# Optimization experiments

Hardware: AMD Instinct MI355X
Metric: run time of the kernel (lower is better)

Reference implementation:

```python
import jax, jax.numpy as jnp
import numpy as np

EMBED_DIM = 1024
HEADS = 16
HEAD_DIM = EMBED_DIM // HEADS


def setup_inputs() -> dict:
    key = jax.random.key(0)
    ks = jax.random.split(key, 9)
    D = EMBED_DIM
    s = 1.0 / np.sqrt(D)
    x = jax.random.normal(ks[0], (4, 2048, D), dtype=jnp.float32)
    Wq = jax.random.uniform(ks[1], (D, D), jnp.float32, -s, s)
    bq = jnp.zeros((D,), jnp.float32)
    Wk = jax.random.uniform(ks[2], (D, D), jnp.float32, -s, s)
    bk = jnp.zeros((D,), jnp.float32)
    Wv = jax.random.uniform(ks[3], (D, D), jnp.float32, -s, s)
    bv = jnp.zeros((D,), jnp.float32)
    Wo = jax.random.uniform(ks[4], (D, D), jnp.float32, -s, s)
    bo = jnp.zeros((D,), jnp.float32)
    gamma = jnp.ones((D,), jnp.float32)
    beta = jnp.zeros((D,), jnp.float32)
    return {"x": x, "Wq": Wq, "bq": bq, "Wk": Wk, "bk": bk,
            "Wv": Wv, "bv": bv, "Wo": Wo, "bo": bo,
            "gamma": gamma, "beta": beta}


def reference(x, Wq, bq, Wk, bk, Wv, bv, Wo, bo, gamma, beta):
    B, S, D = x.shape
    H, Dh = HEADS, HEAD_DIM
    # projections -> [B, H, S, Dh]
    q = (x @ Wq + bq).reshape(B, S, H, Dh).transpose(0, 2, 1, 3)
    k = (x @ Wk + bk).reshape(B, S, H, Dh).transpose(0, 2, 1, 3)
    v = (x @ Wv + bv).reshape(B, S, H, Dh).transpose(0, 2, 1, 3)
    scores = jnp.einsum('bhqd,bhkd->bhqk', q, k) / jnp.sqrt(jnp.float32(Dh))
    attn = jax.nn.softmax(scores, axis=-1)  # dropout is identity in eval
    ctx = jnp.einsum('bhqk,bhkd->bhqd', attn, v)
    ctx = ctx.transpose(0, 2, 1, 3).reshape(B, S, D)
    out = ctx @ Wo + bo
    # residual + LayerNorm (eps=1e-5, torch default)
    h = out + x
    mu = jnp.mean(h, axis=-1, keepdims=True)
    var = jnp.mean(jnp.square(h - mu), axis=-1, keepdims=True)
    return (h - mu) * jax.lax.rsqrt(var + 1e-5) * gamma + beta
```

## Files before the change

### kernel.cpp

```cpp
#include <hip/hip_runtime.h>
#include <hip/hip_bf16.h>
#include <stdint.h>

typedef short sh4 __attribute__((ext_vector_type(4)));
typedef short sh8 __attribute__((ext_vector_type(8)));
typedef float fl4 __attribute__((ext_vector_type(4)));
typedef float f32x4 __attribute__((ext_vector_type(4)));
typedef float f32x16 __attribute__((ext_vector_type(16)));
typedef uint32_t u32x4 __attribute__((ext_vector_type(4)));

static __device__ __forceinline__ short f2bf(float f) {
  union { float f; uint32_t u; } v;
  v.f = f;
  uint32_t r = v.u + 0x7fffu + ((v.u >> 16) & 1u);
  return (short)(r >> 16);
}

static __device__ __forceinline__ uint32_t cvt_pk_bf16(float a, float b) {
  uint32_t r;
  asm("v_cvt_pk_bf16_f32 %0, %1, %2" : "=v"(r) : "v"(a), "v"(b));
  return r;
}

static __device__ __forceinline__ void pl32swap(uint32_t& a, uint32_t& b) {
  asm volatile("v_permlane32_swap_b32 %0, %1" : "+v"(a), "+v"(b));
}

static __device__ __forceinline__ void gload_lds16(const void* g, void* l) {
  __builtin_amdgcn_global_load_lds((const __attribute__((address_space(1))) void*)g,
                                   (__attribute__((address_space(3))) void*)l, 16, 0, 0);
}

__global__ __launch_bounds__(256) void k_wt(const float* __restrict__ Wq, const float* __restrict__ Wk,
                                            const float* __restrict__ Wv, const float* __restrict__ Wo,
                                            short* __restrict__ Tq, short* __restrict__ Tk,
                                            short* __restrict__ Tv, short* __restrict__ To) {
  const float* W = blockIdx.z == 0 ? Wq : blockIdx.z == 1 ? Wk : blockIdx.z == 2 ? Wv : Wo;
  short* T = blockIdx.z == 0 ? Tq : blockIdx.z == 1 ? Tk : blockIdx.z == 2 ? Tv : To;
  __shared__ float tile[32][33];
  int n0 = blockIdx.x * 32, k0 = blockIdx.y * 32;
  int tx = threadIdx.x, ty = threadIdx.y;
#pragma unroll
  for (int p = 0; p < 4; p++) tile[ty + 8 * p][tx] = W[(size_t)(k0 + ty + 8 * p) * 1024 + n0 + tx];
  __syncthreads();
#pragma unroll
  for (int p = 0; p < 4; p++) T[(size_t)(n0 + ty + 8 * p) * 1024 + k0 + tx] = f2bf(tile[tx][ty + 8 * p]);
}

__global__ __launch_bounds__(256) void k_cvtx(const float* __restrict__ x, short* __restrict__ o) {
  int i = blockIdx.x * 256 + threadIdx.x;
  fl4 v = ((const fl4*)x)[i];
  sh4 r;
#pragma unroll
  for (int j = 0; j < 4; j++) r[j] = f2bf(v[j]);
  ((sh4*)o)[i] = r;
}

#define PIPE_LOOP(STAGE_BODY, COMPUTE_BODY, VM)                          \
  STAGE_BODY(0, 0);                                                      \
  STAGE_BODY(1, 1);                                                      \
  {                                                                      \
    int bufc = 0, bufs = 2;                                              \
    for (int it = 0; it < 32; it++) {                                    \
      if (it < 31)                                                       \
        asm volatile("s_waitcnt vmcnt(" VM ")" ::: "memory");            \
      else                                                               \
        asm volatile("s_waitcnt vmcnt(0)" ::: "memory");                 \
      __builtin_amdgcn_s_barrier();                                      \
      if (it + 2 < 32) { STAGE_BODY(it + 2, bufs); }                     \
      __builtin_amdgcn_sched_barrier(0);                                 \
      { int buf = bufc; COMPUTE_BODY }                                   \
      bufc = bufc == 2 ? 0 : bufc + 1;                                   \
      bufs = bufs == 2 ? 0 : bufs + 1;                                   \
      asm volatile("" ::: "memory");                                     \
    }                                                                    \
  }

__global__ __launch_bounds__(512, 4) void k_qk(const short* __restrict__ A, const short* __restrict__ WT2,
                                               const float* __restrict__ bq, const float* __restrict__ bk,
                                               short* __restrict__ Qo, short* __restrict__ Ko, float qscale) {
  __shared__ __align__(16) short As[3][256 * 32];
  __shared__ __align__(16) short Bs[3][128 * 32];
  const int xcd = blockIdx.x & 7, j = blockIdx.x >> 3;
  const int m0 = (j >> 1) * 256, n0 = (xcd * 2 + (j & 1)) * 128;
  const int sec = n0 >> 10;
  const float* bias = sec == 0 ? bq : bk;
  short* Out = sec == 0 ? Qo : Ko;
  const float scale = sec == 0 ? qscale : 1.f;
  const int t = threadIdx.x;
  const int lane = t & 63, w = t >> 6;
  const int wr = w >> 1, wc = w & 1;
  const int l15 = lane & 15, g = lane >> 4;
  f32x4 acc[4][4];
#pragma unroll
  for (int mi = 0; mi < 4; mi++)
#pragma unroll
    for (int ni = 0; ni < 4; ni++) acc[mi][ni] = (f32x4){0.f, 0.f, 0.f, 0.f};

#define QK_STAGE(kt, buf)                                                                     \
  {                                                                                           \
    int r0 = w * 32;                                                                          \
    _Pragma("unroll") for (int i = 0; i < 2; i++) {                                           \
      int row = r0 + i * 16 + (lane >> 2);                                                    \
      gload_lds16(&A[(size_t)(m0 + row) * 1024 + (kt) * 32 + (lane & 3) * 8],                 \
                  &As[buf][(r0 + i * 16) * 32]);                                              \
    }                                                                                         \
    int brow = w * 16 + (lane >> 2);                                                          \
    gload_lds16(&WT2[(size_t)(n0 + brow) * 1024 + (kt) * 32 + (lane & 3) * 8],                \
                &Bs[buf][(w * 16) * 32]);                                                     \
  }

#define QK_COMPUTE                                                                            \
  sh8 a[4], b[4];                                                                             \
  _Pragma("unroll") for (int i = 0; i < 4; i++)                                               \
      a[i] = *(sh8*)&As[buf][(wr * 64 + i * 16 + l15) * 32 + g * 8];                          \
  _Pragma("unroll") for (int i = 0; i < 4; i++)                                               \
      b[i] = *(sh8*)&Bs[buf][(wc * 64 + i * 16 + l15) * 32 + g * 8];                          \
  _Pragma("unroll") for (int mi = 0; mi < 4; mi++)                                            \
      _Pragma("unroll") for (int ni = 0; ni < 4; ni++)                                        \
          acc[mi][ni] = __builtin_amdgcn_mfma_f32_16x16x32_bf16(b[ni], a[mi], acc[mi][ni], 0, 0, 0);

  PIPE_LOOP(QK_STAGE, QK_COMPUTE, "3")

#pragma unroll
  for (int ni = 0; ni < 4; ni++) {
    int nbase = n0 + wc * 64 + ni * 16 + g * 4;
    int nn0 = nbase & 1023;
    fl4 bv4 = *(const fl4*)&bias[nn0];
    int h = nn0 >> 6, dh0 = nn0 & 63;
#pragma unroll
    for (int mi = 0; mi < 4; mi++) {
      int m = m0 + wr * 64 + mi * 16 + l15;
      int bb = m >> 11, s = m & 2047;
      uint2 dd;
      dd.x = cvt_pk_bf16((acc[mi][ni][0] + bv4[0]) * scale, (acc[mi][ni][1] + bv4[1]) * scale);
      dd.y = cvt_pk_bf16((acc[mi][ni][2] + bv4[2]) * scale, (acc[mi][ni][3] + bv4[3]) * scale);
      *(uint2*)&Out[(((size_t)bb * 16 + h) * 2048 + s) * 64 + dh0] = dd;
    }
  }
}

__global__ __launch_bounds__(256) void k_v(const short* __restrict__ A, const short* __restrict__ WTv,
                                           const float* __restrict__ bv, short* __restrict__ Vo) {
  __shared__ __align__(16) short As[3][128 * 32];
  __shared__ __align__(16) short Bs[3][128 * 32];
  const int xcd = blockIdx.x & 7, j = blockIdx.x >> 3;
  const int m0 = (xcd + 8 * (j & 7)) * 128, n0 = (j >> 3) * 128;
  const int t = threadIdx.x;
  const int lane = t & 63, w = t >> 6;
  const int wr = w >> 1, wc = w & 1;
  const int l15 = lane & 15, g = lane >> 4;
  f32x4 acc[4][4];
#pragma unroll
  for (int mi = 0; mi < 4; mi++)
#pragma unroll
    for (int ni = 0; ni < 4; ni++) acc[mi][ni] = (f32x4){0.f, 0.f, 0.f, 0.f};

#define V_STAGE(kt, buf)                                                                      \
  {                                                                                           \
    int r0 = w * 32;                                                                          \
    _Pragma("unroll") for (int i = 0; i < 2; i++) {                                           \
      int row = r0 + i * 16 + (lane >> 2);                                                    \
      gload_lds16(&A[(size_t)(m0 + row) * 1024 + (kt) * 32 + (lane & 3) * 8],                 \
                  &As[buf][(r0 + i * 16) * 32]);                                              \
      gload_lds16(&WTv[(size_t)(n0 + row) * 1024 + (kt) * 32 + (lane & 3) * 8],               \
                  &Bs[buf][(r0 + i * 16) * 32]);                                              \
    }                                                                                         \
  }

#define V_COMPUTE                                                                             \
  sh8 a[4], b[4];                                                                             \
  _Pragma("unroll") for (int i = 0; i < 4; i++)                                               \
      a[i] = *(sh8*)&As[buf][(wr * 64 + i * 16 + l15) * 32 + g * 8];                          \
  _Pragma("unroll") for (int i = 0; i < 4; i++)                                               \
      b[i] = *(sh8*)&Bs[buf][(wc * 64 + i * 16 + l15) * 32 + g * 8];                          \
  _Pragma("unroll") for (int mi = 0; mi < 4; mi++)                                            \
      _Pragma("unroll") for (int ni = 0; ni < 4; ni++)                                        \
          acc[mi][ni] = __builtin_amdgcn_mfma_f32_16x16x32_bf16(a[mi], b[ni], acc[mi][ni], 0, 0, 0);

  PIPE_LOOP(V_STAGE, V_COMPUTE, "4")

#pragma unroll
  for (int ni = 0; ni < 4; ni++) {
    int col = n0 + wc * 64 + ni * 16 + l15;
    int nn = col & 1023;
    float bvv = bv[nn];
    int h = nn >> 6, dh = nn & 63;
#pragma unroll
    for (int mi = 0; mi < 4; mi++) {
      int mr = m0 + wr * 64 + mi * 16 + g * 4;
      int bb = mr >> 11, s = mr & 2047;
      uint2 dd;
      dd.x = cvt_pk_bf16(acc[mi][ni][0] + bvv, acc[mi][ni][1] + bvv);
      dd.y = cvt_pk_bf16(acc[mi][ni][2] + bvv, acc[mi][ni][3] + bvv);
      *(uint2*)&Vo[(((size_t)bb * 16 + h) * 64 + dh) * 2048 + s] = dd;
    }
  }
}

__global__ __launch_bounds__(256) void k_oproj(const short* __restrict__ A, const short* __restrict__ BT,
                                               const float* __restrict__ bias, const float* __restrict__ X,
                                               float* __restrict__ Out) {
  __shared__ __align__(16) short As[3][128 * 32];
  __shared__ __align__(16) short Bs[3][128 * 32];
  const int xcd = blockIdx.x & 7, j = blockIdx.x >> 3;
  const int m0 = (xcd + 8 * (j & 7)) * 128, n0 = (j >> 3) * 128;
  const int t = threadIdx.x;
  const int lane = t & 63, w = t >> 6;
  const int wr = w >> 1, wc = w & 1;
  const int l15 = lane & 15, g = lane >> 4;
  f32x4 acc[4][4];
#pragma unroll
  for (int mi = 0; mi < 4; mi++)
#pragma unroll
    for (int ni = 0; ni < 4; ni++) acc[mi][ni] = (f32x4){0.f, 0.f, 0.f, 0.f};

#define O_STAGE(kt, buf)                                                                      \
  {                                                                                           \
    int r0 = w * 32;                                                                          \
    _Pragma("unroll") for (int i = 0; i < 2; i++) {                                           \
      int row = r0 + i * 16 + (lane >> 2);                                                    \
      gload_lds16(&A[(size_t)(m0 + row) * 1024 + (kt) * 32 + (lane & 3) * 8],                 \
                  &As[buf][(r0 + i * 16) * 32]);                                              \
      gload_lds16(&BT[(size_t)(n0 + row) * 1024 + (kt) * 32 + (lane & 3) * 8],                \
                  &Bs[buf][(r0 + i * 16) * 32]);                                              \
    }                                                                                         \
  }

#define O_COMPUTE                                                                             \
  sh8 a[4], b[4];                                                                             \
  _Pragma("unroll") for (int i = 0; i < 4; i++)                                               \
      a[i] = *(sh8*)&As[buf][(wr * 64 + i * 16 + l15) * 32 + g * 8];                          \
  _Pragma("unroll") for (int i = 0; i < 4; i++)                                               \
      b[i] = *(sh8*)&Bs[buf][(wc * 64 + i * 16 + l15) * 32 + g * 8];                          \
  _Pragma("unroll") for (int mi = 0; mi < 4; mi++)                                            \
      _Pragma("unroll") for (int ni = 0; ni < 4; ni++)                                        \
          acc[mi][ni] = __builtin_amdgcn_mfma_f32_16x16x32_bf16(b[ni], a[mi], acc[mi][ni], 0, 0, 0);

  PIPE_LOOP(O_STAGE, O_COMPUTE, "4")

#pragma unroll
  for (int ni = 0; ni < 4; ni++) {
    int nbase = n0 + wc * 64 + ni * 16 + g * 4;
    fl4 bv4 = *(const fl4*)&bias[nbase];
#pragma unroll
    for (int mi = 0; mi < 4; mi++) {
      int m = m0 + wr * 64 + mi * 16 + l15;
      fl4 xv = *(const fl4*)&X[(size_t)m * 1024 + nbase];
      fl4 r;
#pragma unroll
      for (int e = 0; e < 4; e++) r[e] = acc[mi][ni][e] + bv4[e] + xv[e];
      *(fl4*)&Out[(size_t)m * 1024 + nbase] = r;
    }
  }
}

__global__ __launch_bounds__(512, 4) void k_attn(const short* __restrict__ Q, const short* __restrict__ K,
                                                 const short* __restrict__ Vt, short* __restrict__ CTX) {
  const int nid = (blockIdx.x & 7) * 64 + (blockIdx.x >> 3);
  const int qbi = nid & 7, h = (nid >> 3) & 15, b = nid >> 7;
  const int q0 = qbi * 256;
  const size_t ho = (((size_t)b * 16 + h) * 2048) * 64;
  const short* Qh = Q + ho;
  const short* Kh = K + ho;
  const short* Vh = Vt + ho;
  __shared__ __align__(16) short Ks[3][8 * 512];
  __shared__ __align__(16) short Vs[4][8 * 512];
  const int t = threadIdx.x, lane = t & 63, w = t >> 6;
  const int l31 = lane & 31, hi = lane >> 5;

  sh8 qreg[4];
#pragma unroll
  for (int ks = 0; ks < 4; ks++)
    qreg[ks] = *(const sh8*)&Qh[(size_t)(q0 + w * 32 + l31) * 64 + ks * 16 + hi * 8];

  f32x16 zinit;
#pragma unroll
  for (int r = 0; r < 16; r++) zinit[r] = 0.f;

  f32x16 oc0 = zinit, oc1 = zinit;
  float l_s = 0.f;
  u32x4 pwp[4];

  auto stageK = [&](int kt, int buf) {
    gload_lds16(&Kh[(size_t)(kt * 64 + (w >> 2) * 32 + l31) * 64 + (w & 3) * 16 + hi * 8],
                (char*)&Ks[buf][0] + w * 1024);
  };
  auto stageV = [&](int kt, int buf) {
    gload_lds16(&Vh[(size_t)((w >> 2) * 32 + l31) * 2048 + kt * 64 + (w & 3) * 16 + hi * 8],
                (char*)&Vs[buf][0] + w * 1024);
  };

  stageK(0, 0); stageV(0, 0);
  stageK(1, 1); stageV(1, 1);

  for (int kt = 0; kt < 32; kt++) {
    if (kt < 31)
      asm volatile("s_waitcnt vmcnt(2)" ::: "memory");
    else
      asm volatile("s_waitcnt vmcnt(0)" ::: "memory");
    __builtin_amdgcn_s_barrier();
    if (kt + 2 < 32) { stageK(kt + 2, (kt + 2) % 3); stageV(kt + 2, (kt + 2) & 3); }
    __builtin_amdgcn_sched_barrier(0);
    const int kbuf = kt % 3;

    f32x16 s0, s1;
    __builtin_amdgcn_s_setprio(1);
#pragma unroll
    for (int ks = 0; ks < 4; ks++) {
      sh8 ak0 = *(sh8*)((char*)&Ks[kbuf][0] + ks * 1024 + lane * 16);
      sh8 ak1 = *(sh8*)((char*)&Ks[kbuf][0] + (4 + ks) * 1024 + lane * 16);
      if (ks == 0) {
        s0 = __builtin_amdgcn_mfma_f32_32x32x16_bf16(ak0, qreg[0], zinit, 0, 0, 0);
        s1 = __builtin_amdgcn_mfma_f32_32x32x16_bf16(ak1, qreg[0], zinit, 0, 0, 0);
      } else {
        s0 = __builtin_amdgcn_mfma_f32_32x32x16_bf16(ak0, qreg[ks], s0, 0, 0, 0);
        s1 = __builtin_amdgcn_mfma_f32_32x32x16_bf16(ak1, qreg[ks], s1, 0, 0, 0);
      }
    }

    if (kt > 0) {
      const int vb = (kt - 1) & 3;
#pragma unroll
      for (int ks = 0; ks < 4; ks++) {
        sh8 pb = __builtin_bit_cast(sh8, pwp[ks]);
        sh8 av0 = *(sh8*)((char*)&Vs[vb][0] + ks * 1024 + lane * 16);
        sh8 av1 = *(sh8*)((char*)&Vs[vb][0] + (4 + ks) * 1024 + lane * 16);
        oc0 = __builtin_amdgcn_mfma_f32_32x32x16_bf16(av0, pb, oc0, 0, 0, 0);
        oc1 = __builtin_amdgcn_mfma_f32_32x32x16_bf16(av1, pb, oc1, 0, 0, 0);
      }
    }
    __builtin_amdgcn_s_setprio(0);

    float ps = 0.f;
#pragma unroll
    for (int r = 0; r < 16; r++) { s0[r] = __builtin_amdgcn_exp2f(s0[r]); ps += s0[r]; }
#pragma unroll
    for (int r = 0; r < 16; r++) { s1[r] = __builtin_amdgcn_exp2f(s1[r]); ps += s1[r]; }
    l_s += ps;

    {
      uint32_t a0 = cvt_pk_bf16(s0[0], s0[1]), a1 = cvt_pk_bf16(s0[2], s0[3]);
      uint32_t b0 = cvt_pk_bf16(s0[4], s0[5]), b1 = cvt_pk_bf16(s0[6], s0[7]);
      uint32_t c0 = cvt_pk_bf16(s0[8], s0[9]), c1 = cvt_pk_bf16(s0[10], s0[11]);
      uint32_t d0 = cvt_pk_bf16(s0[12], s0[13]), d1 = cvt_pk_bf16(s0[14], s0[15]);
      pl32swap(a0, b0); pl32swap(a1, b1); pl32swap(c0, d0); pl32swap(c1, d1);
      pwp[0] = (u32x4){a0, a1, b0, b1};
      pwp[1] = (u32x4){c0, c1, d0, d1};
      a0 = cvt_pk_bf16(s1[0], s1[1]); a1 = cvt_pk_bf16(s1[2], s1[3]);
      b0 = cvt_pk_bf16(s1[4], s1[5]); b1 = cvt_pk_bf16(s1[6], s1[7]);
      c0 = cvt_pk_bf16(s1[8], s1[9]); c1 = cvt_pk_bf16(s1[10], s1[11]);
      d0 = cvt_pk_bf16(s1[12], s1[13]); d1 = cvt_pk_bf16(s1[14], s1[15]);
      pl32swap(a0, b0); pl32swap(a1, b1); pl32swap(c0, d0); pl32swap(c1, d1);
      pwp[2] = (u32x4){a0, a1, b0, b1};
      pwp[3] = (u32x4){c0, c1, d0, d1};
    }
    asm volatile("" ::: "memory");
  }

  {
    const int vb = 31 & 3;
    __builtin_amdgcn_s_setprio(1);
#pragma unroll
    for (int ks = 0; ks < 4; ks++) {
      sh8 pb = __builtin_bit_cast(sh8, pwp[ks]);
      sh8 av0 = *(sh8*)((char*)&Vs[vb][0] + ks * 1024 + lane * 16);
      sh8 av1 = *(sh8*)((char*)&Vs[vb][0] + (4 + ks) * 1024 + lane * 16);
      oc0 = __builtin_amdgcn_mfma_f32_32x32x16_bf16(av0, pb, oc0, 0, 0, 0);
      oc1 = __builtin_amdgcn_mfma_f32_32x32x16_bf16(av1, pb, oc1, 0, 0, 0);
    }
    __builtin_amdgcn_s_setprio(0);
  }

  l_s += __shfl_xor(l_s, 32);
  float li = 1.f / l_s;
  int s = q0 + w * 32 + l31;
  size_t obase = (((size_t)b * 2048 + s) * 16 + h) * 64;
#pragma unroll
  for (int rq = 0; rq < 4; rq++) {
    uint2 dd;
    dd.x = cvt_pk_bf16(oc0[4 * rq] * li, oc0[4 * rq + 1] * li);
    dd.y = cvt_pk_bf16(oc0[4 * rq + 2] * li, oc0[4 * rq + 3] * li);
    *(uint2*)&CTX[obase + rq * 8 + hi * 4] = dd;
    dd.x = cvt_pk_bf16(oc1[4 * rq] * li, oc1[4 * rq + 1] * li);
    dd.y = cvt_pk_bf16(oc1[4 * rq + 2] * li, oc1[4 * rq + 3] * li);
    *(uint2*)&CTX[obase + 32 + rq * 8 + hi * 4] = dd;
  }
}

__global__ __launch_bounds__(256) void k_ln(float* __restrict__ Out, const float* __restrict__ gamma,
                                            const float* __restrict__ beta) {
  int row = blockIdx.x * 4 + (threadIdx.x >> 6);
  int lane = threadIdx.x & 63;
  float* p = Out + (size_t)row * 1024;
  fl4 v[4];
  float s = 0.f, s2 = 0.f;
#pragma unroll
  for (int j = 0; j < 4; j++) {
    v[j] = *(fl4*)&p[lane * 4 + j * 256];
#pragma unroll
    for (int e = 0; e < 4; e++) { s += v[j][e]; s2 += v[j][e] * v[j][e]; }
  }
#pragma unroll
  for (int off = 1; off < 64; off <<= 1) {
    s += __shfl_xor(s, off);
    s2 += __shfl_xor(s2, off);
  }
  float mu = s * (1.f / 1024.f);
  float var = s2 * (1.f / 1024.f) - mu * mu;
  float inv = rsqrtf(var + 1e-5f);
#pragma unroll
  for (int j = 0; j < 4; j++) {
    fl4 r;
#pragma unroll
    for (int e = 0; e < 4; e++) {
      int c = lane * 4 + j * 256 + e;
      r[e] = (v[j][e] - mu) * inv * gamma[c] + beta[c];
    }
    *(fl4*)&p[lane * 4 + j * 256] = r;
  }
}

extern "C" void kernel_launch(void* const* d_in, const int* in_sizes, int n_in,
                              void* d_out, int out_size, void* d_ws, size_t ws_size,
                              hipStream_t stream) {
  (void)in_sizes; (void)n_in; (void)out_size; (void)ws_size;
  const float* x = (const float*)d_in[0];
  const float* Wq = (const float*)d_in[1];
  const float* bq = (const float*)d_in[2];
  const float* Wk = (const float*)d_in[3];
  const float* bk = (const float*)d_in[4];
  const float* Wv = (const float*)d_in[5];
  const float* bv = (const float*)d_in[6];
  const float* Wo = (const float*)d_in[7];
  const float* bo = (const float*)d_in[8];
  const float* gamma = (const float*)d_in[9];
  const float* beta = (const float*)d_in[10];
  float* out = (float*)d_out;
  char* ws = (char*)d_ws;
  short* xbf = (short*)(ws);
  short* wtq = (short*)(ws + (16ull << 20));
  short* wtk = (short*)(ws + (18ull << 20));
  short* wtv = (short*)(ws + (20ull << 20));
  short* wto = (short*)(ws + (22ull << 20));
  short* qb  = (short*)(ws + (24ull << 20));
  short* kbuf = (short*)(ws + (40ull << 20));
  short* vbuf = (short*)(ws + (56ull << 20));
  short* ctx = (short*)(ws + (72ull << 20));

  const float QSCALE = 0.125f * 1.44269504088896f;

  k_wt<<<dim3(32, 32, 4), dim3(32, 8), 0, stream>>>(Wq, Wk, Wv, Wo, wtq, wtk, wtv, wto);
  k_cvtx<<<8192, 256, 0, stream>>>(x, xbf);
  k_qk<<<512, 512, 0, stream>>>(xbf, wtq, bq, bk, qb, kbuf, QSCALE);
  k_v<<<512, 256, 0, stream>>>(xbf, wtv, bv, vbuf);
  k_attn<<<512, 512, 0, stream>>>(qb, kbuf, vbuf, ctx);
  k_oproj<<<512, 256, 0, stream>>>(ctx, wto, bo, x, out);
  k_ln<<<2048, 256, 0, stream>>>(out, gamma, beta);
}
```

Before: 206.2 us.

## Merge x conversion into weight transpose kernel and deepen attention K/V prefetch

Folds the fp32-to-bf16 conversion of x into the weight-transpose launch as a fifth grid slice, which removes one kernel launch. In the attention kernel, K/V prefetch depth rises from 2 to 3 tiles, with more LDS buffers and adjusted vmcnt waits, to hide global load latency. The row-sum of exponentials is rewritten as a tree reduction to shorten the dependent add chain. The larger LDS footprint (72KB per block) may reduce occupancy below the requested 4 blocks per CU.

```diff
diff --git a/kernel.cpp b/kernel.cpp
--- a/kernel.cpp
+++ b/kernel.cpp
@@ -34,7 +34,22 @@
 __global__ __launch_bounds__(256) void k_wt(const float* __restrict__ Wq, const float* __restrict__ Wk,
                                             const float* __restrict__ Wv, const float* __restrict__ Wo,
                                             short* __restrict__ Tq, short* __restrict__ Tk,
-                                            short* __restrict__ Tv, short* __restrict__ To) {
+                                            short* __restrict__ Tv, short* __restrict__ To,
+                                            const float* __restrict__ x, short* __restrict__ xbf) {
+  if (blockIdx.z == 4) {
+    int tid = threadIdx.y * 32 + threadIdx.x;
+    size_t base = ((size_t)blockIdx.y * 32 + blockIdx.x) * 8192;
+#pragma unroll
+    for (int i = 0; i < 8; i++) {
+      size_t idx = base + (size_t)i * 1024 + tid * 4;
+      fl4 v = *(const fl4*)&x[idx];
+      sh4 r;
+#pragma unroll
+      for (int j = 0; j < 4; j++) r[j] = f2bf(v[j]);
+      *(sh4*)&xbf[idx] = r;
+    }
+    return;
+  }
   const float* W = blockIdx.z == 0 ? Wq : blockIdx.z == 1 ? Wk : blockIdx.z == 2 ? Wv : Wo;
   short* T = blockIdx.z == 0 ? Tq : blockIdx.z == 1 ? Tk : blockIdx.z == 2 ? Tv : To;
   __shared__ float tile[32][33];
@@ -45,15 +60,6 @@
   __syncthreads();
 #pragma unroll
   for (int p = 0; p < 4; p++) T[(size_t)(n0 + ty + 8 * p) * 1024 + k0 + tx] = f2bf(tile[tx][ty + 8 * p]);
-}
-
-__global__ __launch_bounds__(256) void k_cvtx(const float* __restrict__ x, short* __restrict__ o) {
-  int i = blockIdx.x * 256 + threadIdx.x;
-  fl4 v = ((const fl4*)x)[i];
-  sh4 r;
-#pragma unroll
-  for (int j = 0; j < 4; j++) r[j] = f2bf(v[j]);
-  ((sh4*)o)[i] = r;
 }
 
 #define PIPE_LOOP(STAGE_BODY, COMPUTE_BODY, VM)                          \
@@ -264,8 +270,8 @@
   const short* Qh = Q + ho;
   const short* Kh = K + ho;
   const short* Vh = Vt + ho;
-  __shared__ __align__(16) short Ks[3][8 * 512];
-  __shared__ __align__(16) short Vs[4][8 * 512];
+  __shared__ __align__(16) short Ks[4][8 * 512];
+  __shared__ __align__(16) short Vs[5][8 * 512];
   const int t = threadIdx.x, lane = t & 63, w = t >> 6;
   const int l31 = lane & 31, hi = lane >> 5;
 
@@ -293,16 +299,20 @@
 
   stageK(0, 0); stageV(0, 0);
   stageK(1, 1); stageV(1, 1);
+  stageK(2, 2); stageV(2, 2);
+  int vs = 3, vp = 4;
 
   for (int kt = 0; kt < 32; kt++) {
-    if (kt < 31)
+    if (kt < 30)
+      asm volatile("s_waitcnt vmcnt(4)" ::: "memory");
+    else if (kt == 30)
       asm volatile("s_waitcnt vmcnt(2)" ::: "memory");
     else
       asm volatile("s_waitcnt vmcnt(0)" ::: "memory");
     __builtin_amdgcn_s_barrier();
-    if (kt + 2 < 32) { stageK(kt + 2, (kt + 2) % 3); stageV(kt + 2, (kt + 2) & 3); }
+    if (kt + 3 < 32) { stageK(kt + 3, (kt + 3) & 3); stageV(kt + 3, vs); }
     __builtin_amdgcn_sched_barrier(0);
-    const int kbuf = kt % 3;
+    const int kbuf = kt & 3;
 
     f32x16 s0, s1;
     __builtin_amdgcn_s_setprio(1);
@@ -320,24 +330,29 @@
     }
 
     if (kt > 0) {
-      const int vb = (kt - 1) & 3;
 #pragma unroll
       for (int ks = 0; ks < 4; ks++) {
         sh8 pb = __builtin_bit_cast(sh8, pwp[ks]);
-        sh8 av0 = *(sh8*)((char*)&Vs[vb][0] + ks * 1024 + lane * 16);
-        sh8 av1 = *(sh8*)((char*)&Vs[vb][0] + (4 + ks) * 1024 + lane * 16);
+        sh8 av0 = *(sh8*)((char*)&Vs[vp][0] + ks * 1024 + lane * 16);
+        sh8 av1 = *(sh8*)((char*)&Vs[vp][0] + (4 + ks) * 1024 + lane * 16);
         oc0 = __builtin_amdgcn_mfma_f32_32x32x16_bf16(av0, pb, oc0, 0, 0, 0);
         oc1 = __builtin_amdgcn_mfma_f32_32x32x16_bf16(av1, pb, oc1, 0, 0, 0);
       }
     }
     __builtin_amdgcn_s_setprio(0);
 
-    float ps = 0.f;
-#pragma unroll
-    for (int r = 0; r < 16; r++) { s0[r] = __builtin_amdgcn_exp2f(s0[r]); ps += s0[r]; }
-#pragma unroll
-    for (int r = 0; r < 16; r++) { s1[r] = __builtin_amdgcn_exp2f(s1[r]); ps += s1[r]; }
-    l_s += ps;
+#pragma unroll
+    for (int r = 0; r < 16; r++) s0[r] = __builtin_amdgcn_exp2f(s0[r]);
+#pragma unroll
+    for (int r = 0; r < 16; r++) s1[r] = __builtin_amdgcn_exp2f(s1[r]);
+    {
+      float t0[8];
+#pragma unroll
+      for (int r = 0; r < 8; r++) t0[r] = (s0[2 * r] + s0[2 * r + 1]) + (s1[2 * r] + s1[2 * r + 1]);
+      float u0 = (t0[0] + t0[1]) + (t0[2] + t0[3]);
+      float u1 = (t0[4] + t0[5]) + (t0[6] + t0[7]);
+      l_s += u0 + u1;
+    }
 
     {
       uint32_t a0 = cvt_pk_bf16(s0[0], s0[1]), a1 = cvt_pk_bf16(s0[2], s0[3]);
@@ -355,17 +370,18 @@
       pwp[2] = (u32x4){a0, a1, b0, b1};
       pwp[3] = (u32x4){c0, c1, d0, d1};
     }
+    vp = vp == 4 ? 0 : vp + 1;
+    vs = vs == 4 ? 0 : vs + 1;
     asm volatile("" ::: "memory");
   }
 
   {
-    const int vb = 31 & 3;
     __builtin_amdgcn_s_setprio(1);
 #pragma unroll
     for (int ks = 0; ks < 4; ks++) {
       sh8 pb = __builtin_bit_cast(sh8, pwp[ks]);
-      sh8 av0 = *(sh8*)((char*)&Vs[vb][0] + ks * 1024 + lane * 16);
-      sh8 av1 = *(sh8*)((char*)&Vs[vb][0] + (4 + ks) * 1024 + lane * 16);
+      sh8 av0 = *(sh8*)((char*)&Vs[vp][0] + ks * 1024 + lane * 16);
+      sh8 av1 = *(sh8*)((char*)&Vs[vp][0] + (4 + ks) * 1024 + lane * 16);
       oc0 = __builtin_amdgcn_mfma_f32_32x32x16_bf16(av0, pb, oc0, 0, 0, 0);
       oc1 = __builtin_amdgcn_mfma_f32_32x32x16_bf16(av1, pb, oc1, 0, 0, 0);
     }
@@ -450,8 +466,7 @@
 
   const float QSCALE = 0.125f * 1.44269504088896f;
 
-  k_wt<<<dim3(32, 32, 4), dim3(32, 8), 0, stream>>>(Wq, Wk, Wv, Wo, wtq, wtk, wtv, wto);
-  k_cvtx<<<8192, 256, 0, stream>>>(x, xbf);
+  k_wt<<<dim3(32, 32, 5), dim3(32, 8), 0, stream>>>(Wq, Wk, Wv, Wo, wtq, wtk, wtv, wto, x, xbf);
   k_qk<<<512, 512, 0, stream>>>(xbf, wtq, bq, bk, qb, kbuf, QSCALE);
   k_v<<<512, 256, 0, stream>>>(xbf, wtv, bv, vbuf);
   k_attn<<<512, 512, 0, stream>>>(qb, kbuf, vbuf, ctx);
```

After: 205.0 us. No clear change (-0.6%).
